# Kernel optimization log

Measured on AMD Instinct MI355X. Metric: run time of the kernel, lower is better.

The kernel has to match this reference:

```python
import jax, jax.numpy as jnp
import numpy as np

B, N, M, C = 4, 768, 768, 128
K_NN, K1_NN = 16, 8
NUM_KEYPOINTS = 256
NN_MARGIN = 0.7


def pairwise_distance_batch(x, y):
    # x: (B,C,N), y: (B,C,M) -> squared euclidean distance map (B,N,M)
    xx = jnp.sum(x * x, axis=1)[:, :, None]
    yy = jnp.sum(y * y, axis=1)[:, None, :]
    return xx + yy - 2.0 * jnp.einsum('bcn,bcm->bnm', x, y)


def discriminator(knn_distance, src_knn_distance, w1, b1, w2, b2, w3, b3, w4, b4):
    # inlier-evaluation weight function: pointwise MLP over (B,N,k,6), max-pool over k, MLP -> sigmoid weight (B,1,N)
    x = jnp.concatenate([knn_distance, src_knn_distance], axis=-1)  # (B,N,k,6)
    h = jax.nn.relu(jnp.einsum('bnkc,oc->bnko', x, w1) + b1)
    h = jax.nn.relu(jnp.einsum('bnko,po->bnkp', h, w2) + b2)
    g = h.max(axis=2)  # (B,N,64) pool over neighbors
    g = jax.nn.relu(jnp.einsum('bnp,qp->bnq', g, w3) + b3)
    w = jax.nn.sigmoid(jnp.einsum('bnq,rq->bnr', g, w4) + b4)  # (B,N,1)
    return w.transpose(0, 2, 1)  # (B,1,N)


def compute_rigid_transformation(src, src_corr, weight):
    # weighted Kabsch/SVD rigid fit. src/src_corr: (B,3,N), weight: (B,1,N)
    w = weight / (jnp.sum(weight, axis=2, keepdims=True) + 1e-8)
    src_mean = jnp.sum(src * w, axis=2, keepdims=True)
    corr_mean = jnp.sum(src_corr * w, axis=2, keepdims=True)
    src_c = (src - src_mean) * w
    corr_c = src_corr - corr_mean
    H = jnp.einsum('bin,bjn->bij', src_c, corr_c)  # (B,3,3)
    U, S, Vt = jnp.linalg.svd(H)
    V = Vt.transpose(0, 2, 1)
    det = jnp.linalg.det(jnp.einsum('bij,bkj->bik', V, U))  # det(V U^T)
    d = jnp.stack([jnp.ones_like(det), jnp.ones_like(det), det], axis=-1)  # (B,3)
    R = jnp.einsum('bij,bj,bkj->bik', V, d, U)
    t = corr_mean - jnp.einsum('bij,bjk->bik', R, src_mean)  # (B,3,1)
    return R, t


def _forward(src, tgt, src_embedding, tgt_embedding, src_idx, k, src_knn, i, tgt_knn, src_idx1, idx2, k1,
             w1, b1, w2, b2, w3, b3, w4, b4, num_keypoints, nn_margin):
    Bs, _, Ns = src.shape
    Ms = tgt.shape[2]
    dist = pairwise_distance_batch(src_embedding, tgt_embedding)  # (B,N,M)
    scores = jax.nn.softmax(-dist, axis=2)
    # neighborhood consensus: sum_{a>=1,c>=1} scores[b, nbr_src(i,a), nbr_tgt(j,c)] / (k1-1)
    S1 = scores.reshape(Bs * Ns, Ms)[src_idx1].reshape(Bs, Ns, k1, Ms)  # gather src-neighbor rows
    A = jnp.sum(S1[:, :, 1:, :], axis=2)  # (B,N,M), drop self (a=0)
    idx2c = idx2[:, :, 1:]  # (B,M,k1-1), drop self (c=0)
    consensus = jax.vmap(lambda a, idx: jnp.sum(a[:, idx], axis=-1))(A, idx2c) / (k1 - 1)  # (B,N,M)
    src_knn_scores = nn_margin - consensus
    refined = jnp.exp(src_knn_scores) * dist
    matching = jax.nn.softmax(-refined, axis=2)  # refined matching map (B,N,M)
    src_corr = jnp.einsum('bcm,bnm->bcn', tgt, matching)  # soft correspondences (B,3,N)
    src_corr_t = src_corr.transpose(0, 2, 1)  # (B,N,3)
    src_knn_corr = src_corr_t.reshape(Bs * Ns, 3)[src_idx].reshape(Bs, Ns, k, 3)
    knn_distance = src_corr_t[:, :, None, :] - src_knn_corr  # (B,N,k,3)
    src_knn_distance = src.transpose(0, 2, 1)[:, :, None, :] - src_knn
    weight = discriminator(knn_distance, src_knn_distance, w1, b1, w2, b2, w3, b3, w4, b4)  # (B,1,N)
    R, t = compute_rigid_transformation(src, src_corr, weight)
    _, topk_idx = jax.lax.top_k(weight[:, 0, :], num_keypoints)  # (B,K)
    bidx = jnp.arange(Bs)[:, None]
    bc = jnp.broadcast_to(topk_idx[:, None, :], (Bs, 3, num_keypoints))
    src_keypoints = jnp.take_along_axis(src, bc, axis=2)  # (B,3,K)
    tgt_keypoints = jnp.take_along_axis(src_corr, bc, axis=2)
    idx_tgt_corr = jnp.argmax(matching, axis=-1)  # (B,N)
    kp_corr = jnp.take_along_axis(idx_tgt_corr, topk_idx, axis=1)  # (B,K)
    keypoints_one_hot = jax.nn.one_hot(kp_corr, Ms, dtype=matching.dtype)  # (B,K,M)
    pred_scores = matching[bidx, topk_idx]  # (B,K,M)
    loss_scl = jnp.mean(jnp.sum(-jnp.log(pred_scores + 1e-15) * keypoints_one_hot, axis=-1))
    tgt_keypoints_knn = knn_distance[bidx, topk_idx].transpose(0, 3, 1, 2)  # (B,3,K,k)
    src_transformed = jnp.einsum('bij,bjn->bin', R, src) + t
    st = src_transformed.transpose(0, 2, 1)  # (B,N,3)
    st_knn_corr = st.reshape(Bs * Ns, 3)[src_idx].reshape(Bs, Ns, k, 3)
    knn_distance2 = st[:, :, None, :] - st_knn_corr
    src_keypoints_knn = knn_distance2[bidx, topk_idx].transpose(0, 3, 1, 2)  # (B,3,K,k)
    return (R, t.reshape(Bs, 3), src_keypoints, tgt_keypoints, src_keypoints_knn, tgt_keypoints_knn, loss_scl)


def setup_inputs() -> dict:
    key = jax.random.key(0)
    ks = jax.random.split(key, 12)
    src = jax.random.normal(ks[0], (B, 3, N), jnp.float32)
    tgt = jax.random.normal(ks[1], (B, 3, M), jnp.float32)
    src_embedding = jax.random.normal(ks[2], (B, C, N), jnp.float32)
    tgt_embedding = jax.random.normal(ks[3], (B, C, M), jnp.float32)
    # knn index lists; first neighbor is the point itself (matching the [:,:,1:] self-exclusion slices)
    idxk = jax.random.randint(ks[4], (B, N, K_NN), 0, N).at[:, :, 0].set(jnp.arange(N)[None, :])
    idxk1 = jax.random.randint(ks[5], (B, N, K1_NN), 0, N).at[:, :, 0].set(jnp.arange(N)[None, :])
    idx2 = jax.random.randint(ks[6], (B, M, K1_NN), 0, M).at[:, :, 0].set(jnp.arange(M)[None, :])
    off = jnp.arange(B)[:, None, None] * N
    src_idx = (idxk + off).reshape(-1)   # flat indices into (B*N) rows
    src_idx1 = (idxk1 + off).reshape(-1)
    bidx = jnp.arange(B)[:, None, None]
    src_knn = src.transpose(0, 2, 1)[bidx, idxk]   # (B,N,k,3) coords of neighbors
    tgt_knn = tgt.transpose(0, 2, 1)[bidx, idx2]   # (B,M,k1,3) (unused by forward, kept for signature fidelity)
    s = 0.1
    w1 = jax.random.normal(ks[7], (64, 6), jnp.float32) * s
    w2 = jax.random.normal(ks[8], (64, 64), jnp.float32) * s
    w3 = jax.random.normal(ks[9], (32, 64), jnp.float32) * s
    w4 = jax.random.normal(ks[10], (1, 32), jnp.float32) * s
    return {"src": src, "tgt": tgt, "src_embedding": src_embedding, "tgt_embedding": tgt_embedding,
            "src_idx": src_idx, "k": K_NN, "src_knn": src_knn, "i": 0, "tgt_knn": tgt_knn,
            "src_idx1": src_idx1, "idx2": idx2, "k1": K1_NN,
            "w1": w1, "b1": jnp.zeros((64,), jnp.float32), "w2": w2, "b2": jnp.zeros((64,), jnp.float32),
            "w3": w3, "b3": jnp.zeros((32,), jnp.float32), "w4": w4, "b4": jnp.zeros((1,), jnp.float32),
            "num_keypoints": NUM_KEYPOINTS, "nn_margin": NN_MARGIN}


def reference(src, tgt, src_embedding, tgt_embedding, src_idx, k, src_knn, i, tgt_knn, src_idx1, idx2, k1,
              w1, b1, w2, b2, w3, b3, w4, b4, num_keypoints, nn_margin):
    return _forward(src, tgt, src_embedding, tgt_embedding, src_idx, k, src_knn, i, tgt_knn, src_idx1, idx2, k1,
                    w1, b1, w2, b2, w3, b3, w4, b4, num_keypoints, nn_margin)
```

## Files before the change

kernel.cpp:

```cpp
#include <hip/hip_runtime.h>
#include <hip/hip_bf16.h>
#include <math.h>

#define BB 4
#define NN 768
#define MM 768
#define CC 128
#define KK 16
#define KK1 8
#define NKP 256

#define OFF_R    0
#define OFF_T    36
#define OFF_SK   48
#define OFF_TK   3120
#define OFF_SKK  6192
#define OFF_TKK  55344
#define OFF_LOSS 104496

__global__ __launch_bounds__(256) void dist_k(const float* __restrict__ xe,
                                              const float* __restrict__ ye,
                                              float* __restrict__ dist) {
    __shared__ float xt[CC * 64];
    __shared__ float yt[CC * 64];
    __shared__ float nx[64];
    __shared__ float ny[64];
    int b = blockIdx.z, n0 = blockIdx.y * 64, m0 = blockIdx.x * 64;
    int tid = threadIdx.x;
    for (int i = tid; i < CC * 16; i += 256) {
        int c = i >> 4, v = i & 15;
        ((float4*)xt)[c * 16 + v] = ((const float4*)(xe + (size_t)(b * CC + c) * NN + n0))[v];
        ((float4*)yt)[c * 16 + v] = ((const float4*)(ye + (size_t)(b * CC + c) * MM + m0))[v];
    }
    __syncthreads();
    if (tid < 64) {
        float s = 0.f;
        for (int c = 0; c < CC; c++) { float v = xt[c * 64 + tid]; s += v * v; }
        nx[tid] = s;
    } else if (tid < 128) {
        int v0 = tid - 64;
        float s = 0.f;
        for (int c = 0; c < CC; c++) { float v = yt[c * 64 + v0]; s += v * v; }
        ny[v0] = s;
    }
    int mi = (tid & 15) * 4, ni = (tid >> 4) * 4;
    float acc[16];
    for (int k = 0; k < 16; k++) acc[k] = 0.f;
    for (int c = 0; c < CC; c++) {
        float4 xv = *(const float4*)&xt[c * 64 + ni];
        float4 yv = *(const float4*)&yt[c * 64 + mi];
        acc[0]  += xv.x * yv.x; acc[1]  += xv.x * yv.y; acc[2]  += xv.x * yv.z; acc[3]  += xv.x * yv.w;
        acc[4]  += xv.y * yv.x; acc[5]  += xv.y * yv.y; acc[6]  += xv.y * yv.z; acc[7]  += xv.y * yv.w;
        acc[8]  += xv.z * yv.x; acc[9]  += xv.z * yv.y; acc[10] += xv.z * yv.z; acc[11] += xv.z * yv.w;
        acc[12] += xv.w * yv.x; acc[13] += xv.w * yv.y; acc[14] += xv.w * yv.z; acc[15] += xv.w * yv.w;
    }
    __syncthreads();
    float ny0 = ny[mi], ny1 = ny[mi + 1], ny2 = ny[mi + 2], ny3 = ny[mi + 3];
    for (int i = 0; i < 4; i++) {
        float nxi = nx[ni + i];
        float4 o;
        o.x = nxi + ny0 - 2.f * acc[i * 4 + 0];
        o.y = nxi + ny1 - 2.f * acc[i * 4 + 1];
        o.z = nxi + ny2 - 2.f * acc[i * 4 + 2];
        o.w = nxi + ny3 - 2.f * acc[i * 4 + 3];
        *(float4*)&dist[((size_t)b * NN + n0 + ni + i) * MM + m0 + mi] = o;
    }
}

__global__ __launch_bounds__(256) void stats_k(const float* __restrict__ dist,
                                               float* __restrict__ rowstats) {
    int tid = threadIdx.x;
    int lane = tid & 63, wv = tid >> 6;
    int r = blockIdx.x * 4 + wv;
    const float* dr = dist + (size_t)r * MM;
    float4 v4[3];
    float mn = 1e30f;
    for (int q = 0; q < 3; q++) {
        v4[q] = *(const float4*)&dr[256 * q + lane * 4];
        mn = fminf(mn, fminf(fminf(v4[q].x, v4[q].y), fminf(v4[q].z, v4[q].w)));
    }
    for (int off = 32; off >= 1; off >>= 1) mn = fminf(mn, __shfl_down(mn, off));
    mn = __shfl(mn, 0);
    float z = 0.f;
    for (int q = 0; q < 3; q++) {
        z += expf(mn - v4[q].x) + expf(mn - v4[q].y) + expf(mn - v4[q].z) + expf(mn - v4[q].w);
    }
    for (int off = 32; off >= 1; off >>= 1) z += __shfl_down(z, off);
    if (lane == 0) { rowstats[2 * r] = mn; rowstats[2 * r + 1] = 1.0f / z; }
}

__global__ __launch_bounds__(256) void match_k(const float* __restrict__ dist,
                                               const float* __restrict__ rowstats,
                                               const int* __restrict__ src_idx1,
                                               const int* __restrict__ idx2,
                                               const float* __restrict__ tgt,
                                               const float* __restrict__ nn_margin_p,
                                               float* __restrict__ src_corr,
                                               float* __restrict__ mmax) {
    __shared__ float ArowAll[4 * MM];
    int tid = threadIdx.x;
    int lane = tid & 63, wv = tid >> 6;
    int r = blockIdx.x * 4 + wv;
    int b = r / NN, n = r % NN;
    float* Arow = ArowAll + wv * MM;
    int rows[KK1 - 1];
    float mnj[KK1 - 1], izj[KK1 - 1];
    for (int j = 0; j < KK1 - 1; j++) {
        rows[j] = src_idx1[r * KK1 + 1 + j];
        mnj[j] = rowstats[2 * rows[j]];
        izj[j] = rowstats[2 * rows[j] + 1];
    }
    float4 a4[3];
    for (int q = 0; q < 3; q++) a4[q] = make_float4(0.f, 0.f, 0.f, 0.f);
    for (int j = 0; j < KK1 - 1; j++) {
        const float* dj = dist + (size_t)rows[j] * MM;
        float mj = mnj[j], iz = izj[j];
        for (int q = 0; q < 3; q++) {
            float4 d = *(const float4*)&dj[256 * q + lane * 4];
            a4[q].x += expf(mj - d.x) * iz;
            a4[q].y += expf(mj - d.y) * iz;
            a4[q].z += expf(mj - d.z) * iz;
            a4[q].w += expf(mj - d.w) * iz;
        }
    }
    for (int q = 0; q < 3; q++)
        *(float4*)&Arow[256 * q + lane * 4] = a4[q];
    __syncthreads();
    float marg = nn_margin_p[0];
    const float* drow = dist + (size_t)r * MM;
    float4 rv4[3];
    float mn = 1e30f;
    for (int q = 0; q < 3; q++) {
        int mbase = 256 * q + lane * 4;
        float4 d = *(const float4*)&drow[mbase];
        float rr[4];
        for (int c = 0; c < 4; c++) {
            int m = mbase + c;
            const int4* ip = (const int4*)(idx2 + ((size_t)b * MM + m) * KK1);
            int4 i0 = ip[0], i1 = ip[1];
            float cons = Arow[i0.y] + Arow[i0.z] + Arow[i0.w] +
                         Arow[i1.x] + Arow[i1.y] + Arow[i1.z] + Arow[i1.w];
            float dc = (c == 0) ? d.x : (c == 1) ? d.y : (c == 2) ? d.z : d.w;
            rr[c] = expf(marg - cons * (1.0f / (KK1 - 1))) * dc;
            mn = fminf(mn, rr[c]);
        }
        rv4[q] = make_float4(rr[0], rr[1], rr[2], rr[3]);
    }
    for (int off = 32; off >= 1; off >>= 1) mn = fminf(mn, __shfl_down(mn, off));
    mn = __shfl(mn, 0);
    float z = 0.f, s0 = 0.f, s1 = 0.f, s2 = 0.f;
    const float* t0 = tgt + (size_t)b * 3 * MM;
    for (int q = 0; q < 3; q++) {
        int mbase = 256 * q + lane * 4;
        float4 ta = *(const float4*)&t0[mbase];
        float4 tb = *(const float4*)&t0[MM + mbase];
        float4 tc = *(const float4*)&t0[2 * MM + mbase];
        float4 e4;
        e4.x = expf(mn - rv4[q].x); e4.y = expf(mn - rv4[q].y);
        e4.z = expf(mn - rv4[q].z); e4.w = expf(mn - rv4[q].w);
        z  += e4.x + e4.y + e4.z + e4.w;
        s0 += e4.x * ta.x + e4.y * ta.y + e4.z * ta.z + e4.w * ta.w;
        s1 += e4.x * tb.x + e4.y * tb.y + e4.z * tb.z + e4.w * tb.w;
        s2 += e4.x * tc.x + e4.y * tc.y + e4.z * tc.z + e4.w * tc.w;
    }
    for (int off = 32; off >= 1; off >>= 1) {
        z += __shfl_down(z, off); s0 += __shfl_down(s0, off);
        s1 += __shfl_down(s1, off); s2 += __shfl_down(s2, off);
    }
    if (lane == 0) {
        float inv = 1.0f / z;
        src_corr[(size_t)(b * 3 + 0) * NN + n] = s0 * inv;
        src_corr[(size_t)(b * 3 + 1) * NN + n] = s1 * inv;
        src_corr[(size_t)(b * 3 + 2) * NN + n] = s2 * inv;
        mmax[r] = inv;
    }
}

__global__ __launch_bounds__(256) void disc_k(const float* __restrict__ src,
                                              const float* __restrict__ src_corr,
                                              const float* __restrict__ src_knn,
                                              const int* __restrict__ src_idx,
                                              const float* __restrict__ w1, const float* __restrict__ b1,
                                              const float* __restrict__ w2, const float* __restrict__ b2,
                                              const float* __restrict__ w3, const float* __restrict__ b3,
                                              const float* __restrict__ w4, const float* __restrict__ b4,
                                              float* __restrict__ knnD, float* __restrict__ wgt) {
    __shared__ float w1s[64 * 7];
    __shared__ float w2s[64 * 65];
    __shared__ float w3s[32 * 65];
    __shared__ float xs[4][16 * 6];
    __shared__ float h1s[4][16 * 64];
    __shared__ float gs[4][64];
    int tid = threadIdx.x;
    for (int i = tid; i < 64 * 6; i += 256) w1s[(i / 6) * 7 + (i % 6)] = w1[i];
    for (int i = tid; i < 64 * 64; i += 256) w2s[(i / 64) * 65 + (i % 64)] = w2[i];
    for (int i = tid; i < 32 * 64; i += 256) w3s[(i / 64) * 65 + (i % 64)] = w3[i];
    int w = tid >> 6, l = tid & 63;
    int r = blockIdx.x * 4 + w;
    int b = r / NN, n = r % NN;
    if (l < KK) {
        int j = l;
        int f = src_idx[r * KK + j];
        int fb = f / NN, fn = f % NN;
        for (int c = 0; c < 3; c++) {
            float scn = src_corr[(size_t)(b * 3 + c) * NN + n];
            float kd = scn - src_corr[(size_t)(fb * 3 + c) * NN + fn];
            xs[w][j * 6 + c] = kd;
            knnD[((size_t)r * KK + j) * 3 + c] = kd;
            float sd = src[(size_t)(b * 3 + c) * NN + n] - src_knn[((size_t)r * KK + j) * 3 + c];
            xs[w][j * 6 + 3 + c] = sd;
        }
    }
    __syncthreads();
    float bb1 = b1[l];
    for (int k = 0; k < KK; k++) {
        float h = bb1;
        for (int c = 0; c < 6; c++) h += xs[w][k * 6 + c] * w1s[l * 7 + c];
        h1s[w][k * 64 + l] = h > 0.f ? h : 0.f;
    }
    __syncthreads();
    float bb2 = b2[l];
    float acc2[KK];
    for (int k = 0; k < KK; k++) acc2[k] = bb2;
    for (int o4 = 0; o4 < 16; o4++) {
        float wa = w2s[l * 65 + o4 * 4 + 0];
        float wb = w2s[l * 65 + o4 * 4 + 1];
        float wc = w2s[l * 65 + o4 * 4 + 2];
        float wd = w2s[l * 65 + o4 * 4 + 3];
        for (int k = 0; k < KK; k++) {
            float4 h = *(const float4*)&h1s[w][k * 64 + o4 * 4];
            acc2[k] += h.x * wa + h.y * wb + h.z * wc + h.w * wd;
        }
    }
    float gm = 0.f;
    for (int k = 0; k < KK; k++) gm = fmaxf(gm, acc2[k]);
    gs[w][l] = gm;
    __syncthreads();
    float val = 0.f;
    if (l < 32) {
        float h = b3[l];
        for (int o = 0; o < 64; o++) h += gs[w][o] * w3s[l * 65 + o];
        h = h > 0.f ? h : 0.f;
        val = h * w4[l];
    }
    for (int off = 32; off >= 1; off >>= 1) val += __shfl_down(val, off);
    if (l == 0) wgt[r] = 1.0f / (1.0f + expf(-(val + b4[0])));
}

__global__ __launch_bounds__(256) void rigidtopk_k(const float* __restrict__ src,
                                                   const float* __restrict__ src_corr,
                                                   const float* __restrict__ wgt,
                                                   float* __restrict__ out,
                                                   float* __restrict__ Rws, float* __restrict__ tws,
                                                   int* __restrict__ topk,
                                                   float* __restrict__ lossAcc) {
    int tid = threadIdx.x;
    int lane = tid & 63, wv = tid >> 6;
    if (blockIdx.x < 48) {
        __shared__ float wl[NN];
        int job = blockIdx.x;
        int bx = job % 12, b = job / 12;
        for (int i = tid; i < NN; i += 256) wl[i] = wgt[b * NN + i];
        __syncthreads();
        int i = bx * 64 + (tid >> 2);
        int q = tid & 3;
        float v = wl[i];
        int rank = 0;
        for (int t = 0; t < NN / 4; t++) {
            int j = q + 4 * t;
            float u = wl[j];
            rank += (u > v) || (u == v && j < i);
        }
        rank += __shfl_down(rank, 2, 4);
        rank += __shfl_down(rank, 1, 4);
        if (q == 0 && rank < NKP) topk[b * NKP + rank] = i;
        return;
    }
    __shared__ double redd[BB * 16];
    int b = wv;
    double acc[16];
    for (int k = 0; k < 16; k++) acc[k] = 0.0;
    for (int n = lane; n < NN; n += 64) {
        double wvv = wgt[b * NN + n];
        double s[3], q[3];
        for (int i = 0; i < 3; i++) {
            s[i] = src[(size_t)(b * 3 + i) * NN + n];
            q[i] = src_corr[(size_t)(b * 3 + i) * NN + n];
        }
        acc[0] += wvv;
        for (int i = 0; i < 3; i++) acc[1 + i] += wvv * s[i];
        for (int j = 0; j < 3; j++) acc[4 + j] += wvv * q[j];
        for (int i = 0; i < 3; i++)
            for (int j = 0; j < 3; j++) acc[7 + i * 3 + j] += wvv * s[i] * q[j];
    }
    for (int k = 0; k < 16; k++)
        for (int off = 32; off >= 1; off >>= 1) acc[k] += __shfl_down(acc[k], off);
    if (lane == 0)
        for (int k = 0; k < 16; k++) redd[b * 16 + k] = acc[k];
    __syncthreads();
    if (tid == 0) { lossAcc[0] = 0.f; ((int*)lossAcc)[1] = 0; }
    if (tid >= BB) return;
    int bb = tid;
    const double* S = redd + bb * 16;
    double T = S[0], D = T + 1e-8;
    double sm[3], cm[3];
    for (int i = 0; i < 3; i++) { sm[i] = S[1 + i] / D; cm[i] = S[4 + i] / D; }
    double fac = 2.0 - T / D;
    double H[3][3];
    for (int i = 0; i < 3; i++)
        for (int j = 0; j < 3; j++) H[i][j] = S[7 + i * 3 + j] / D - sm[i] * cm[j] * fac;
    double Sxx = H[0][0], Sxy = H[0][1], Sxz = H[0][2];
    double Syx = H[1][0], Syy = H[1][1], Syz = H[1][2];
    double Szx = H[2][0], Szy = H[2][1], Szz = H[2][2];
    double A[4][4];
    A[0][0] = Sxx + Syy + Szz; A[0][1] = Syz - Szy;        A[0][2] = Szx - Sxz;        A[0][3] = Sxy - Syx;
    A[1][0] = A[0][1];         A[1][1] = Sxx - Syy - Szz;  A[1][2] = Sxy + Syx;        A[1][3] = Szx + Sxz;
    A[2][0] = A[0][2];         A[2][1] = A[1][2];          A[2][2] = -Sxx + Syy - Szz; A[2][3] = Syz + Szy;
    A[3][0] = A[0][3];         A[3][1] = A[1][3];          A[3][2] = A[2][3];          A[3][3] = -Sxx - Syy + Szz;
    double V[4][4] = {{1,0,0,0},{0,1,0,0},{0,0,1,0},{0,0,0,1}};
    for (int sweep = 0; sweep < 15; sweep++) {
        double offd = A[0][1]*A[0][1] + A[0][2]*A[0][2] + A[0][3]*A[0][3]
                    + A[1][2]*A[1][2] + A[1][3]*A[1][3] + A[2][3]*A[2][3];
        if (offd < 1e-26) break;
        for (int p = 0; p < 3; p++) {
            for (int q = p + 1; q < 4; q++) {
                double apq = A[p][q];
                if (fabs(apq) < 1e-60) continue;
                double theta = 0.5 * (A[q][q] - A[p][p]) / apq;
                double t = (theta >= 0 ? 1.0 : -1.0) / (fabs(theta) + sqrt(theta * theta + 1.0));
                double c = 1.0 / sqrt(t * t + 1.0), s = t * c;
                for (int k = 0; k < 4; k++) {
                    double akp = A[k][p], akq = A[k][q];
                    A[k][p] = c * akp - s * akq; A[k][q] = s * akp + c * akq;
                }
                for (int k = 0; k < 4; k++) {
                    double apk = A[p][k], aqk = A[q][k];
                    A[p][k] = c * apk - s * aqk; A[q][k] = s * apk + c * aqk;
                }
                for (int k = 0; k < 4; k++) {
                    double vkp = V[k][p], vkq = V[k][q];
                    V[k][p] = c * vkp - s * vkq; V[k][q] = s * vkp + c * vkq;
                }
            }
        }
    }
    int best = 0;
    for (int k = 1; k < 4; k++) if (A[k][k] > A[best][best]) best = k;
    double qw = V[0][best], qx = V[1][best], qy = V[2][best], qz = V[3][best];
    double nq = sqrt(qw * qw + qx * qx + qy * qy + qz * qz);
    qw /= nq; qx /= nq; qy /= nq; qz /= nq;
    double R[3][3];
    R[0][0] = 1 - 2 * (qy * qy + qz * qz); R[0][1] = 2 * (qx * qy - qw * qz); R[0][2] = 2 * (qx * qz + qw * qy);
    R[1][0] = 2 * (qx * qy + qw * qz); R[1][1] = 1 - 2 * (qx * qx + qz * qz); R[1][2] = 2 * (qy * qz - qw * qx);
    R[2][0] = 2 * (qx * qz - qw * qy); R[2][1] = 2 * (qy * qz + qw * qx); R[2][2] = 1 - 2 * (qx * qx + qy * qy);
    for (int i = 0; i < 3; i++)
        for (int j = 0; j < 3; j++) {
            out[OFF_R + bb * 9 + i * 3 + j] = (float)R[i][j];
            Rws[bb * 9 + i * 3 + j] = (float)R[i][j];
        }
    for (int i = 0; i < 3; i++) {
        double tv = cm[i] - (R[i][0] * sm[0] + R[i][1] * sm[1] + R[i][2] * sm[2]);
        out[OFF_T + bb * 3 + i] = (float)tv;
        tws[bb * 3 + i] = (float)tv;
    }
}

__global__ __launch_bounds__(256) void gather_k(const float* __restrict__ src,
                                                const float* __restrict__ src_corr,
                                                const float* __restrict__ knnD,
                                                const int* __restrict__ src_idx,
                                                const int* __restrict__ topk,
                                                const float* __restrict__ Rws,
                                                const float* __restrict__ tws,
                                                const float* __restrict__ mmax,
                                                float* __restrict__ lossAcc,
                                                float* __restrict__ out) {
    __shared__ float lred[4];
    int tid = threadIdx.x;
    int lane = tid & 63, wv = tid >> 6;
    int t = blockIdx.x * 256 + tid;
    int j = t % KK; int br = t / KK; int r = br % NKP; int b = br / NKP;
    int idx = topk[b * NKP + r];
    int rr = b * NN + idx;
    for (int c = 0; c < 3; c++)
        out[OFF_TKK + (size_t)((b * 3 + c) * NKP + r) * KK + j] = knnD[((size_t)rr * KK + j) * 3 + c];
    int f = src_idx[rr * KK + j];
    int fb = f / NN, fn = f % NN;
    float Rb[9], tb[3], Rf[9], tf[3];
    for (int c = 0; c < 9; c++) { Rb[c] = Rws[b * 9 + c]; Rf[c] = Rws[fb * 9 + c]; }
    for (int c = 0; c < 3; c++) { tb[c] = tws[b * 3 + c]; tf[c] = tws[fb * 3 + c]; }
    float sp[3], sf[3];
    for (int c = 0; c < 3; c++) {
        sp[c] = src[(size_t)(b * 3 + c) * NN + idx];
        sf[c] = src[(size_t)(fb * 3 + c) * NN + fn];
    }
    for (int c = 0; c < 3; c++) {
        float sti = Rb[c*3] * sp[0] + Rb[c*3+1] * sp[1] + Rb[c*3+2] * sp[2] + tb[c];
        float stf = Rf[c*3] * sf[0] + Rf[c*3+1] * sf[1] + Rf[c*3+2] * sf[2] + tf[c];
        out[OFF_SKK + (size_t)((b * 3 + c) * NKP + r) * KK + j] = sti - stf;
    }
    float term = 0.f;
    if (j == 0) {
        for (int c = 0; c < 3; c++) {
            out[OFF_SK + (b * 3 + c) * NKP + r] = sp[c];
            out[OFF_TK + (b * 3 + c) * NKP + r] = src_corr[(size_t)(b * 3 + c) * NN + idx];
        }
        term = -logf(mmax[rr] + 1e-15f);
    }
    for (int off = 32; off >= 1; off >>= 1) term += __shfl_down(term, off);
    if (lane == 0) lred[wv] = term;
    __syncthreads();
    if (tid == 0) {
        float bsum = lred[0] + lred[1] + lred[2] + lred[3];
        atomicAdd(&lossAcc[0], bsum);
        __threadfence();
        int old = atomicAdd((int*)&lossAcc[1], 1);
        if (old == (int)gridDim.x - 1) {
            float fin = atomicAdd(&lossAcc[0], 0.f);
            out[OFF_LOSS] = fin / (float)(BB * NKP);
        }
    }
}

extern "C" void kernel_launch(void* const* d_in, const int* in_sizes, int n_in,
                              void* d_out, int out_size, void* d_ws, size_t ws_size,
                              hipStream_t stream) {
    (void)in_sizes; (void)n_in; (void)out_size; (void)ws_size;
    const float* src      = (const float*)d_in[0];
    const float* tgt      = (const float*)d_in[1];
    const float* se       = (const float*)d_in[2];
    const float* te       = (const float*)d_in[3];
    const int*   src_idx  = (const int*)d_in[4];
    const float* src_knn  = (const float*)d_in[6];
    const int*   src_idx1 = (const int*)d_in[9];
    const int*   idx2     = (const int*)d_in[10];
    const float* w1 = (const float*)d_in[12];
    const float* b1 = (const float*)d_in[13];
    const float* w2 = (const float*)d_in[14];
    const float* b2 = (const float*)d_in[15];
    const float* w3 = (const float*)d_in[16];
    const float* b3 = (const float*)d_in[17];
    const float* w4 = (const float*)d_in[18];
    const float* b4 = (const float*)d_in[19];
    const float* nn_margin = (const float*)d_in[21];
    float* out = (float*)d_out;

    float* ws = (float*)d_ws;
    float* dist     = ws;
    float* rowstats = dist + (size_t)BB * NN * MM;
    float* src_corr = rowstats + BB * NN * 2;
    float* mmax     = src_corr + BB * 3 * NN;
    float* knnD     = mmax + BB * NN;
    float* wgt      = knnD + (size_t)BB * NN * KK * 3;
    float* Rws      = wgt + BB * NN;
    float* tws      = Rws + BB * 9;
    int*   topk     = (int*)(tws + BB * 3);
    float* lossAcc  = (float*)(topk + BB * NKP);

    dist_k<<<dim3(MM / 64, NN / 64, BB), 256, 0, stream>>>(se, te, dist);
    stats_k<<<BB * NN / 4, 256, 0, stream>>>(dist, rowstats);
    match_k<<<BB * NN / 4, 256, 0, stream>>>(dist, rowstats, src_idx1, idx2, tgt, nn_margin,
                                             src_corr, mmax);
    disc_k<<<BB * NN / 4, 256, 0, stream>>>(src, src_corr, src_knn, src_idx,
                                            w1, b1, w2, b2, w3, b3, w4, b4, knnD, wgt);
    rigidtopk_k<<<49, 256, 0, stream>>>(src, src_corr, wgt, out, Rws, tws, topk, lossAcc);
    gather_k<<<BB * NKP * KK / 256, 256, 0, stream>>>(src, src_corr, knnD, src_idx, topk,
                                                      Rws, tws, mmax, lossAcc, out);
}
```

Baseline: 184.7 us.

## Fuse row-min into distance kernel, drop stats kernel, register-shuffle discriminator MLP

The distance kernel now writes per-tile row minima, which removes the separate stats kernel launch and its full pass over the distance matrix. The match kernel reduces these partial minima and recomputes each neighbour row's softmax normaliser inline, so that work is repeated across the rows that share a neighbour. The discriminator MLP now keeps hidden activations in registers and exchanges them with wave shuffles, replacing shared-memory staging and two block barriers at the cost of many shuffle instructions and more register pressure.

```diff
diff --git a/kernel.cpp b/kernel.cpp
--- a/kernel.cpp
+++ b/kernel.cpp
@@ -20,7 +20,8 @@
 
 __global__ __launch_bounds__(256) void dist_k(const float* __restrict__ xe,
                                               const float* __restrict__ ye,
-                                              float* __restrict__ dist) {
+                                              float* __restrict__ dist,
+                                              float* __restrict__ rowminPart) {
     __shared__ float xt[CC * 64];
     __shared__ float yt[CC * 64];
     __shared__ float nx[64];
@@ -64,33 +65,15 @@
         o.z = nxi + ny2 - 2.f * acc[i * 4 + 2];
         o.w = nxi + ny3 - 2.f * acc[i * 4 + 3];
         *(float4*)&dist[((size_t)b * NN + n0 + ni + i) * MM + m0 + mi] = o;
-    }
-}
-
-__global__ __launch_bounds__(256) void stats_k(const float* __restrict__ dist,
-                                               float* __restrict__ rowstats) {
-    int tid = threadIdx.x;
-    int lane = tid & 63, wv = tid >> 6;
-    int r = blockIdx.x * 4 + wv;
-    const float* dr = dist + (size_t)r * MM;
-    float4 v4[3];
-    float mn = 1e30f;
-    for (int q = 0; q < 3; q++) {
-        v4[q] = *(const float4*)&dr[256 * q + lane * 4];
-        mn = fminf(mn, fminf(fminf(v4[q].x, v4[q].y), fminf(v4[q].z, v4[q].w)));
-    }
-    for (int off = 32; off >= 1; off >>= 1) mn = fminf(mn, __shfl_down(mn, off));
-    mn = __shfl(mn, 0);
-    float z = 0.f;
-    for (int q = 0; q < 3; q++) {
-        z += expf(mn - v4[q].x) + expf(mn - v4[q].y) + expf(mn - v4[q].z) + expf(mn - v4[q].w);
-    }
-    for (int off = 32; off >= 1; off >>= 1) z += __shfl_down(z, off);
-    if (lane == 0) { rowstats[2 * r] = mn; rowstats[2 * r + 1] = 1.0f / z; }
+        float rmin = fminf(fminf(o.x, o.y), fminf(o.z, o.w));
+        for (int off = 8; off >= 1; off >>= 1) rmin = fminf(rmin, __shfl_down(rmin, off, 16));
+        if ((tid & 15) == 0)
+            rowminPart[(size_t)(b * NN + n0 + ni + i) * 12 + blockIdx.x] = rmin;
+    }
 }
 
 __global__ __launch_bounds__(256) void match_k(const float* __restrict__ dist,
-                                               const float* __restrict__ rowstats,
+                                               const float* __restrict__ rowminPart,
                                                const int* __restrict__ src_idx1,
                                                const int* __restrict__ idx2,
                                                const float* __restrict__ tgt,
@@ -103,24 +86,27 @@
     int r = blockIdx.x * 4 + wv;
     int b = r / NN, n = r % NN;
     float* Arow = ArowAll + wv * MM;
-    int rows[KK1 - 1];
-    float mnj[KK1 - 1], izj[KK1 - 1];
-    for (int j = 0; j < KK1 - 1; j++) {
-        rows[j] = src_idx1[r * KK1 + 1 + j];
-        mnj[j] = rowstats[2 * rows[j]];
-        izj[j] = rowstats[2 * rows[j] + 1];
-    }
     float4 a4[3];
     for (int q = 0; q < 3; q++) a4[q] = make_float4(0.f, 0.f, 0.f, 0.f);
     for (int j = 0; j < KK1 - 1; j++) {
-        const float* dj = dist + (size_t)rows[j] * MM;
-        float mj = mnj[j], iz = izj[j];
+        int rj = src_idx1[r * KK1 + 1 + j];
+        const float* mp = rowminPart + (size_t)rj * 12;
+        float mj = mp[0];
+        for (int t = 1; t < 12; t++) mj = fminf(mj, mp[t]);
+        const float* dj = dist + (size_t)rj * MM;
+        float4 e[3];
+        float zj = 0.f;
         for (int q = 0; q < 3; q++) {
             float4 d = *(const float4*)&dj[256 * q + lane * 4];
-            a4[q].x += expf(mj - d.x) * iz;
-            a4[q].y += expf(mj - d.y) * iz;
-            a4[q].z += expf(mj - d.z) * iz;
-            a4[q].w += expf(mj - d.w) * iz;
+            e[q].x = expf(mj - d.x); e[q].y = expf(mj - d.y);
+            e[q].z = expf(mj - d.z); e[q].w = expf(mj - d.w);
+            zj += e[q].x + e[q].y + e[q].z + e[q].w;
+        }
+        for (int off = 32; off >= 1; off >>= 1) zj += __shfl_down(zj, off);
+        float iz = 1.0f / __shfl(zj, 0);
+        for (int q = 0; q < 3; q++) {
+            a4[q].x += e[q].x * iz; a4[q].y += e[q].y * iz;
+            a4[q].z += e[q].z * iz; a4[q].w += e[q].w * iz;
         }
     }
     for (int q = 0; q < 3; q++)
@@ -188,60 +174,58 @@
     __shared__ float w1s[64 * 7];
     __shared__ float w2s[64 * 65];
     __shared__ float w3s[32 * 65];
-    __shared__ float xs[4][16 * 6];
-    __shared__ float h1s[4][16 * 64];
-    __shared__ float gs[4][64];
     int tid = threadIdx.x;
     for (int i = tid; i < 64 * 6; i += 256) w1s[(i / 6) * 7 + (i % 6)] = w1[i];
     for (int i = tid; i < 64 * 64; i += 256) w2s[(i / 64) * 65 + (i % 64)] = w2[i];
     for (int i = tid; i < 32 * 64; i += 256) w3s[(i / 64) * 65 + (i % 64)] = w3[i];
-    int w = tid >> 6, l = tid & 63;
-    int r = blockIdx.x * 4 + w;
+    int l = tid & 63, wv = tid >> 6;
+    int r = blockIdx.x * 4 + wv;
     int b = r / NN, n = r % NN;
+    float xd0 = 0.f, xd1 = 0.f, xd2 = 0.f, sd0 = 0.f, sd1 = 0.f, sd2 = 0.f;
     if (l < KK) {
         int j = l;
         int f = src_idx[r * KK + j];
         int fb = f / NN, fn = f % NN;
+        float kd[3];
         for (int c = 0; c < 3; c++) {
             float scn = src_corr[(size_t)(b * 3 + c) * NN + n];
-            float kd = scn - src_corr[(size_t)(fb * 3 + c) * NN + fn];
-            xs[w][j * 6 + c] = kd;
-            knnD[((size_t)r * KK + j) * 3 + c] = kd;
-            float sd = src[(size_t)(b * 3 + c) * NN + n] - src_knn[((size_t)r * KK + j) * 3 + c];
-            xs[w][j * 6 + 3 + c] = sd;
-        }
-    }
-    __syncthreads();
+            kd[c] = scn - src_corr[(size_t)(fb * 3 + c) * NN + fn];
+            knnD[((size_t)r * KK + j) * 3 + c] = kd[c];
+        }
+        xd0 = kd[0]; xd1 = kd[1]; xd2 = kd[2];
+        sd0 = src[(size_t)(b * 3 + 0) * NN + n] - src_knn[((size_t)r * KK + j) * 3 + 0];
+        sd1 = src[(size_t)(b * 3 + 1) * NN + n] - src_knn[((size_t)r * KK + j) * 3 + 1];
+        sd2 = src[(size_t)(b * 3 + 2) * NN + n] - src_knn[((size_t)r * KK + j) * 3 + 2];
+    }
+    __syncthreads();
+    float w1r[6];
+    for (int c = 0; c < 6; c++) w1r[c] = w1s[l * 7 + c];
     float bb1 = b1[l];
+    float hreg[KK];
     for (int k = 0; k < KK; k++) {
-        float h = bb1;
-        for (int c = 0; c < 6; c++) h += xs[w][k * 6 + c] * w1s[l * 7 + c];
-        h1s[w][k * 64 + l] = h > 0.f ? h : 0.f;
-    }
-    __syncthreads();
+        float h = bb1
+            + __shfl(xd0, k) * w1r[0] + __shfl(xd1, k) * w1r[1] + __shfl(xd2, k) * w1r[2]
+            + __shfl(sd0, k) * w1r[3] + __shfl(sd1, k) * w1r[4] + __shfl(sd2, k) * w1r[5];
+        hreg[k] = h > 0.f ? h : 0.f;
+    }
+    float acc2[KK];
     float bb2 = b2[l];
-    float acc2[KK];
     for (int k = 0; k < KK; k++) acc2[k] = bb2;
-    for (int o4 = 0; o4 < 16; o4++) {
-        float wa = w2s[l * 65 + o4 * 4 + 0];
-        float wb = w2s[l * 65 + o4 * 4 + 1];
-        float wc = w2s[l * 65 + o4 * 4 + 2];
-        float wd = w2s[l * 65 + o4 * 4 + 3];
-        for (int k = 0; k < KK; k++) {
-            float4 h = *(const float4*)&h1s[w][k * 64 + o4 * 4];
-            acc2[k] += h.x * wa + h.y * wb + h.z * wc + h.w * wd;
-        }
+    for (int o = 0; o < 64; o++) {
+        float w = w2s[l * 65 + o];
+        for (int k = 0; k < KK; k++) acc2[k] += w * __shfl(hreg[k], o);
     }
     float gm = 0.f;
     for (int k = 0; k < KK; k++) gm = fmaxf(gm, acc2[k]);
-    gs[w][l] = gm;
-    __syncthreads();
     float val = 0.f;
+    float h3 = (l < 32) ? b3[l] : 0.f;
+    for (int o = 0; o < 64; o++) {
+        float gv = __shfl(gm, o);
+        if (l < 32) h3 += gv * w3s[l * 65 + o];
+    }
     if (l < 32) {
-        float h = b3[l];
-        for (int o = 0; o < 64; o++) h += gs[w][o] * w3s[l * 65 + o];
-        h = h > 0.f ? h : 0.f;
-        val = h * w4[l];
+        h3 = h3 > 0.f ? h3 : 0.f;
+        val = h3 * w4[l];
     }
     for (int off = 32; off >= 1; off >>= 1) val += __shfl_down(val, off);
     if (l == 0) wgt[r] = 1.0f / (1.0f + expf(-(val + b4[0])));
@@ -446,20 +430,19 @@
     float* out = (float*)d_out;
 
     float* ws = (float*)d_ws;
-    float* dist     = ws;
-    float* rowstats = dist + (size_t)BB * NN * MM;
-    float* src_corr = rowstats + BB * NN * 2;
-    float* mmax     = src_corr + BB * 3 * NN;
-    float* knnD     = mmax + BB * NN;
-    float* wgt      = knnD + (size_t)BB * NN * KK * 3;
-    float* Rws      = wgt + BB * NN;
-    float* tws      = Rws + BB * 9;
-    int*   topk     = (int*)(tws + BB * 3);
-    float* lossAcc  = (float*)(topk + BB * NKP);
-
-    dist_k<<<dim3(MM / 64, NN / 64, BB), 256, 0, stream>>>(se, te, dist);
-    stats_k<<<BB * NN / 4, 256, 0, stream>>>(dist, rowstats);
-    match_k<<<BB * NN / 4, 256, 0, stream>>>(dist, rowstats, src_idx1, idx2, tgt, nn_margin,
+    float* dist        = ws;
+    float* rowminPart  = dist + (size_t)BB * NN * MM;
+    float* src_corr    = rowminPart + (size_t)BB * NN * 12;
+    float* mmax        = src_corr + BB * 3 * NN;
+    float* knnD        = mmax + BB * NN;
+    float* wgt         = knnD + (size_t)BB * NN * KK * 3;
+    float* Rws         = wgt + BB * NN;
+    float* tws         = Rws + BB * 9;
+    int*   topk        = (int*)(tws + BB * 3);
+    float* lossAcc     = (float*)(topk + BB * NKP);
+
+    dist_k<<<dim3(MM / 64, NN / 64, BB), 256, 0, stream>>>(se, te, dist, rowminPart);
+    match_k<<<BB * NN / 4, 256, 0, stream>>>(dist, rowminPart, src_idx1, idx2, tgt, nn_margin,
                                              src_corr, mmax);
     disc_k<<<BB * NN / 4, 256, 0, stream>>>(src, src_corr, src_knn, src_idx,
                                             w1, b1, w2, b2, w3, b3, w4, b4, knnD, wgt);
```

Measured after the change: 209.8 us. 1.14x slower.
